# Kernel optimization log

Hardware: AMD Instinct MI355X
Metric: run time of the kernel (lower is better)

The kernel has to match this reference:

```python
import jax, jax.numpy as jnp
import numpy as np

TAU = 2.0          # gumbel-softmax temperature (module default)
NUM_GROUPS = 2
NUM_VARS = 320
EPS = 1e-7


def setup_inputs() -> dict:
    key = jax.random.key(0)
    k1, k2, k3, k4 = jax.random.split(key, 4)
    B, S, D = 32, 2048, 512
    GK = NUM_GROUPS * NUM_VARS            # 640
    dpg = 256 // NUM_GROUPS               # codevector_dim // num_groups = 128
    hidden_states = jax.random.normal(k1, (B, S, D), dtype=jnp.float32)
    mask_time_indices = jnp.ones((B, S), dtype=bool)
    gumbel_noise = jax.random.gumbel(k2, (B * S * NUM_GROUPS, NUM_VARS), dtype=jnp.float32)
    W = jax.random.normal(k3, (GK, D), dtype=jnp.float32) * (1.0 / np.sqrt(D))
    b = jnp.zeros((GK,), dtype=jnp.float32)
    codevectors = jax.random.uniform(k4, (1, GK, dpg), dtype=jnp.float32)
    return {"hidden_states": hidden_states, "mask_time_indices": mask_time_indices,
            "gumbel_noise": gumbel_noise, "W": W, "b": b, "codevectors": codevectors}


def reference(hidden_states, mask_time_indices, gumbel_noise, W, b, codevectors):
    B, S, D = hidden_states.shape
    G, K = NUM_GROUPS, NUM_VARS
    N = B * S

    # linear projection to logits: (B,S,G*K)
    logits = jnp.einsum('bsd,kd->bsk', hidden_states, W) + b
    logits_flat = logits.reshape(N * G, K)

    # training path: gumbel-softmax with hard straight-through
    y_soft = jax.nn.softmax((logits_flat + gumbel_noise) / TAU, axis=-1)
    idx = jnp.argmax(y_soft, axis=-1)
    y_hard = jax.nn.one_hot(idx, K, dtype=y_soft.dtype)
    probs = y_hard + y_soft - jax.lax.stop_gradient(y_soft)   # (N*G, K)

    # perplexity over the plain (no-gumbel) softmax distribution
    soft_dist = jax.nn.softmax(logits_flat.reshape(N, G, K), axis=-1)
    m = mask_time_indices.reshape(-1)[:, None, None]
    marginal = jnp.where(m, soft_dist, 0.0).sum(axis=0) / mask_time_indices.sum()   # (G, K)
    perplexity = jnp.exp(-jnp.sum(marginal * jnp.log(marginal + EPS), axis=-1)).sum()

    # weighted sum of codevectors per group (avoids (N, G*K, d) intermediate)
    cv = codevectors.reshape(G, K, -1)                         # (G, K, d/G)
    out = jnp.einsum('ngk,gkd->ngd', probs.reshape(N, G, K), cv).reshape(B, S, -1)
    return out, perplexity
```

## Files before the change

### kernel.cpp

```cpp
#include <hip/hip_runtime.h>


#define GG   2
#define KK   320
#define NN   65536
#define DD   512
#define DPG  128
#define EPSL 1e-7f
#define NCPY 8
#define BUFB 24576

typedef __attribute__((ext_vector_type(8))) short bf16x8;
typedef __attribute__((ext_vector_type(4))) float f32x4;
typedef __attribute__((address_space(1))) void glb_void;
typedef __attribute__((address_space(3))) void lds_void;

static __device__ __forceinline__ unsigned short f2bf_rne(float f) {
    unsigned u = __float_as_uint(f);
    u += 0x7FFFu + ((u >> 16) & 1u);
    return (unsigned short)(u >> 16);
}

static __device__ __forceinline__ bf16x8 pack8_rne(float4 v0, float4 v1) {
    union { unsigned short s[8]; bf16x8 b; } u;
    u.s[0] = f2bf_rne(v0.x); u.s[1] = f2bf_rne(v0.y);
    u.s[2] = f2bf_rne(v0.z); u.s[3] = f2bf_rne(v0.w);
    u.s[4] = f2bf_rne(v1.x); u.s[5] = f2bf_rne(v1.y);
    u.s[6] = f2bf_rne(v1.z); u.s[7] = f2bf_rne(v1.w);
    return u.b;
}

static __device__ __forceinline__ unsigned ordf(float f) {
    unsigned u = __float_as_uint(f);
    return (u & 0x80000000u) ? ~u : (u | 0x80000000u);
}

__global__ __launch_bounds__(256) void prep_all(
    const float* __restrict__ H, short* __restrict__ Hbf,
    const float* __restrict__ W, short* __restrict__ Wf,
    float* __restrict__ marg, const int* __restrict__ mask,
    float* __restrict__ cnt_out, int* __restrict__ done)
{
    const int b = blockIdx.x, tid = threadIdx.x;
    if (b < 16384) {
        const int F = b * 4 + (tid >> 6);
        const int l = tid & 63;
        const int tile = F >> 5, f = F & 31;
        const int rf = f >> 4, t = f & 15;
        const int row = tile * 32 + rf * 16 + (l >> 2);
        const float* src = H + (size_t)row * DD + t * 32 + (l & 3) * 8;
        float4 v0 = *(const float4*)src;
        float4 v1 = *(const float4*)(src + 4);
        union { unsigned short s[8]; int d[4]; } u;
        u.s[0] = f2bf_rne(v0.x); u.s[1] = f2bf_rne(v0.y);
        u.s[2] = f2bf_rne(v0.z); u.s[3] = f2bf_rne(v0.w);
        u.s[4] = f2bf_rne(v1.x); u.s[5] = f2bf_rne(v1.y);
        u.s[6] = f2bf_rne(v1.z); u.s[7] = f2bf_rne(v1.w);
        const int ls4 = (4 * (l & 15) + (l >> 4)) * 4;
        int4 o;
        o.x = __builtin_amdgcn_ds_bpermute(ls4, u.d[0]);
        o.y = __builtin_amdgcn_ds_bpermute(ls4, u.d[1]);
        o.z = __builtin_amdgcn_ds_bpermute(ls4, u.d[2]);
        o.w = __builtin_amdgcn_ds_bpermute(ls4, u.d[3]);
        *(int4*)(Hbf + (size_t)F * 512 + (size_t)l * 8) = o;
    } else if (b < 16544) {
        int gt = (b - 16384) * 256 + tid;
        int w  = gt >> 6, l = gt & 63;
        int col = 16 * (w >> 4) + (l & 15);
        int k0  = 32 * (w & 15) + 8 * (l >> 4);
        const float* src = W + (size_t)col * DD + k0;
        float4 v0 = *(const float4*)(src);
        float4 v1 = *(const float4*)(src + 4);
        *(bf16x8*)(Wf + (size_t)w * 512 + (size_t)l * 8) = pack8_rne(v0, v1);
    } else {
        __shared__ float red[256];
        for (int i = tid; i < NCPY * GG * KK; i += 256) marg[i] = 0.f;
        if (tid == 0) *done = 0;
        int c = 0;
        for (int n = tid; n < NN; n += 256) c += (mask[n] != 0) ? 1 : 0;
        red[tid] = (float)c;
        __syncthreads();
        for (int s = 128; s > 0; s >>= 1) {
            if (tid < s) red[tid] += red[tid + s];
            __syncthreads();
        }
        if (tid == 0) *cnt_out = red[0];
    }
}

__global__ __launch_bounds__(512, 4) void vq_main(
    const short* Hbf, const int* __restrict__ mask,
    const float* __restrict__ gumbel, const short* __restrict__ Wf,
    const float* __restrict__ bias, const float* __restrict__ cv,
    int* __restrict__ idxW, float* marg,
    int fused, float* __restrict__ out,
    const float* __restrict__ cnt_in, int* done, float* __restrict__ perp_out)
{
    __shared__ __align__(16) char smem[3 * BUFB];
    __shared__ float    red_s[256];
    __shared__ unsigned red_k[256];
    __shared__ float    wrowS[64];
    __shared__ int      idxf[64];
    __shared__ int      lastflag;

    const int tid = threadIdx.x;
    const int l   = tid & 63, wid = tid >> 6;
    const int rh  = wid >> 2, hc = wid & 3;
    const int g   = blockIdx.x & 1;
    const int T   = blockIdx.x >> 1;
    const int n0  = T * 64;
    const int q   = l >> 4,  ln = l & 15;

    const short* gsrc0[3];
#pragma unroll
    for (int j = 0; j < 3; ++j) {
        const int k = wid * 3 + j;
        if (k < 4) gsrc0[j] = Hbf + (size_t)((2 * T + (k >> 1)) * 32 + (k & 1) * 16) * 512 + (size_t)l * 8;
        else       gsrc0[j] = Wf  + (size_t)((g * 20 + (k - 4)) * 16) * 512 + (size_t)l * 8;
    }

#define ISSUE(t_, b_)                                                          \
    { _Pragma("unroll")                                                        \
      for (int j = 0; j < 3; ++j) {                                            \
          const int k = wid * 3 + j;                                           \
          const short* gsrc = (const short*)((const char*)gsrc0[j] + ((t_) << 10)); \
          char* ldst = smem + (b_)*BUFB + k * 1024;                            \
          __builtin_amdgcn_global_load_lds((const glb_void*)gsrc, (lds_void*)ldst, 16, 0, 0); \
      } }

    f32x4 acc[2][5];
    const f32x4 vzero = {0.f, 0.f, 0.f, 0.f};
#pragma unroll
    for (int a = 0; a < 2; ++a)
#pragma unroll
        for (int b = 0; b < 5; ++b) acc[a][b] = vzero;

#define COMPUTE(b_)                                                            \
    { const char* bb_ = smem + (b_)*BUFB;                                      \
      bf16x8 Ar[2], Br[5];                                                     \
      _Pragma("unroll")                                                        \
      for (int rf = 0; rf < 2; ++rf)                                           \
          Ar[rf] = *(const bf16x8*)(bb_ + (rh * 2 + rf) * 1024 + l * 16);      \
      _Pragma("unroll")                                                        \
      for (int cf = 0; cf < 5; ++cf)                                           \
          Br[cf] = *(const bf16x8*)(bb_ + 4096 + (hc * 5 + cf) * 1024 + l * 16); \
      __builtin_amdgcn_s_setprio(1);                                           \
      _Pragma("unroll")                                                        \
      for (int cf = 0; cf < 5; ++cf) {                                         \
          acc[0][cf] = __builtin_amdgcn_mfma_f32_16x16x32_bf16(Ar[0], Br[cf], acc[0][cf], 0, 0, 0); \
          acc[1][cf] = __builtin_amdgcn_mfma_f32_16x16x32_bf16(Ar[1], Br[cf], acc[1][cf], 0, 0, 0); } \
      __builtin_amdgcn_s_setprio(0); }

    ISSUE(0, 0)
#pragma unroll 1
    for (int c = 0; c < 15; ++c) {
        ISSUE(c + 1, (c + 1) % 3)
        asm volatile("s_waitcnt vmcnt(3)" ::: "memory");
        __builtin_amdgcn_sched_barrier(0);
        __builtin_amdgcn_s_barrier();
        COMPUTE(c % 3)
    }
    asm volatile("s_waitcnt vmcnt(0)" ::: "memory");
    __builtin_amdgcn_sched_barrier(0);
    __builtin_amdgcn_s_barrier();
    COMPUTE(0)

    float bb[5];
#pragma unroll
    for (int cf = 0; cf < 5; ++cf) bb[cf] = bias[g * KK + hc * 80 + 16 * cf + ln];

    float gum[8][5];
#pragma unroll
    for (int rf = 0; rf < 2; ++rf)
#pragma unroll
        for (int reg = 0; reg < 4; ++reg) {
            const int row = 32 * rh + 16 * rf + 4 * q + reg;
            const float* gp = gumbel + ((size_t)(n0 + row) * GG + g) * KK + hc * 80 + ln;
#pragma unroll
            for (int cf = 0; cf < 5; ++cf) gum[rf * 4 + reg][cf] = gp[16 * cf];
        }
    __builtin_amdgcn_sched_barrier(0);

#pragma unroll
    for (int cf = 0; cf < 5; ++cf)
#pragma unroll
        for (int rf = 0; rf < 2; ++rf) {
            acc[rf][cf][0] += bb[cf]; acc[rf][cf][1] += bb[cf];
            acc[rf][cf][2] += bb[cf]; acc[rf][cf][3] += bb[cf];
        }

#pragma unroll
    for (int rf = 0; rf < 2; ++rf) {
#pragma unroll
        for (int reg = 0; reg < 4; ++reg) {
            const int row = 32 * rh + 16 * rf + 4 * q + reg;
            float s = 0.f, zm = -3.0e38f;
            int zi = 0;
#pragma unroll
            for (int cf = 0; cf < 5; ++cf) {
                float v = acc[rf][cf][reg];
                float z = v + gum[rf * 4 + reg][cf];
                if (z > zm) { zm = z; zi = hc * 80 + 16 * cf + ln; }
                float e = __expf(v);
                s += e;
                acc[rf][cf][reg] = e;
            }
            unsigned key = (ordf(zm) & 0xFFFFFE00u) | (unsigned)(511 - zi);
#pragma unroll
            for (int d = 1; d <= 8; d <<= 1) {
                s += __shfl_xor(s, d);
                unsigned ko = (unsigned)__shfl_xor((int)key, d);
                key = key > ko ? key : ko;
            }
            if (ln == 0) {
                const int base = row * 4 + hc;
                red_s[base] = s;
                red_k[base] = key;
            }
        }
    }
    __syncthreads();

    if (tid < 64) {
        const int b0 = tid * 4;
        float Z = red_s[b0] + red_s[b0 + 1] + red_s[b0 + 2] + red_s[b0 + 3];
        unsigned km = red_k[b0];
        km = km > red_k[b0 + 1] ? km : red_k[b0 + 1];
        km = km > red_k[b0 + 2] ? km : red_k[b0 + 2];
        km = km > red_k[b0 + 3] ? km : red_k[b0 + 3];
        const int ib = 511 - (int)(km & 511u);
        idxf[tid]  = ib;
        if (!fused) idxW[(size_t)(n0 + tid) * GG + g] = ib;
        wrowS[tid] = ((mask[n0 + tid] != 0) ? 1.0f : 0.0f) / Z;
    }
    __syncthreads();

    float cs[5] = {0.f, 0.f, 0.f, 0.f, 0.f};
#pragma unroll
    for (int rf = 0; rf < 2; ++rf) {
#pragma unroll
        for (int reg = 0; reg < 4; ++reg) {
            const int row = 32 * rh + 16 * rf + 4 * q + reg;
            const float wv = wrowS[row];
#pragma unroll
            for (int cf = 0; cf < 5; ++cf)
                cs[cf] += acc[rf][cf][reg] * wv;
        }
    }
    {
        float* mc = marg + (size_t)(blockIdx.x & (NCPY - 1)) * (GG * KK);
#pragma unroll
        for (int cf = 0; cf < 5; ++cf) {
            float v = cs[cf];
            v += __shfl_xor(v, 16);
            v += __shfl_xor(v, 32);
            if (l < 16) atomicAdd(&mc[g * KK + hc * 80 + 16 * cf + l], v);
        }
    }

    if (fused) {
#pragma unroll
        for (int i = 0; i < 4; ++i) {
            const int e = tid + 512 * i;
            const int row = e >> 5, d4 = e & 31;
            const float4 v = ((const float4*)cv)[((size_t)g * KK + idxf[row]) * 32 + d4];
            ((float4*)(out + (size_t)(n0 + row) * 256 + g * DPG))[d4] = v;
        }
    }

    asm volatile("s_waitcnt vmcnt(0)" ::: "memory");
    __syncthreads();
    if (tid == 0) {
        int old = atomicAdd(done, 1);
        lastflag = (old == 2047) ? 1 : 0;
    }
    __syncthreads();
    if (lastflag) {
        const float invc = 1.0f / cnt_in[0];
        float hg[GG];
#pragma unroll
        for (int gg = 0; gg < GG; ++gg) {
            float h = 0.f;
            for (int c = tid; c < KK; c += 512) {
                float m = 0.f;
#pragma unroll
                for (int x = 0; x < NCPY; ++x)
                    m += atomicAdd(&marg[x * (GG * KK) + gg * KK + c], 0.0f);
                m *= invc;
                h += m * logf(m + EPSL);
            }
#pragma unroll
            for (int d = 1; d < 64; d <<= 1) h += __shfl_xor(h, d);
            if (l == 0) red_s[wid] = h;
            __syncthreads();
            if (tid == 0) {
                float t = 0.f;
                for (int wv = 0; wv < 8; ++wv) t += red_s[wv];
                red_s[64 + gg] = t;
            }
            __syncthreads();
            hg[gg] = red_s[64 + gg];
        }
        if (tid == 0) perp_out[0] = expf(-hg[0]) + expf(-hg[1]);
    }
}

__global__ __launch_bounds__(256) void gather_kernel(
    const int* __restrict__ idxW, const float* __restrict__ cv,
    float* __restrict__ out)
{
    const int e = blockIdx.x * 256 + threadIdx.x;
    const int n = e >> 6, s4 = e & 63, g = s4 >> 5, d4 = s4 & 31;
    const int idx = idxW[(size_t)n * GG + g];
    const float4 v = ((const float4*)cv)[((size_t)g * KK + idx) * 32 + d4];
    ((float4*)out)[e] = v;
}

extern "C" void kernel_launch(void* const* d_in, const int* in_sizes, int n_in,
                              void* d_out, int out_size, void* d_ws, size_t ws_size,
                              hipStream_t stream)
{
    const float* H      = (const float*)d_in[0];
    const int*   mask   = (const int*)d_in[1];
    const float* gumbel = (const float*)d_in[2];
    const float* W      = (const float*)d_in[3];
    const float* bias   = (const float*)d_in[4];
    const float* cv     = (const float*)d_in[5];

    float*  out  = (float*)d_out;
    float*  marg = (float*)d_ws;
    float*  cnt  = (float*)((char*)d_ws + 24576);
    int*    done = (int*)((char*)d_ws + 24580);
    short*  Wf   = (short*)((char*)d_ws + 32768);
    int*    idxW = (int*)((char*)d_ws + 32768 + 655360);

    const size_t hbf_off  = 2 * 1024 * 1024;
    const size_t hbf_need = hbf_off + (size_t)64 * 1024 * 1024;
    const int fused = (ws_size >= hbf_need) ? 1 : 0;
    short* Hbf = fused ? (short*)((char*)d_ws + hbf_off) : (short*)d_out;

    prep_all<<<16545, 256, 0, stream>>>(H, Hbf, W, Wf, marg, mask, cnt, done);
    vq_main<<<2048, 512, 0, stream>>>(Hbf, mask, gumbel, Wf, bias, cv, idxW, marg,
                                      fused, out, cnt, done,
                                      out + (size_t)NN * GG * DPG);
    if (!fused)
        gather_kernel<<<16384, 256, 0, stream>>>(idxW, cv, out);
}
```

Measured before the change: 164.7 us.

## Store bf16 hidden states row-major and gather MFMA fragments with strided loads

```diff
diff --git a/kernel.cpp b/kernel.cpp
--- a/kernel.cpp
+++ b/kernel.cpp
@@ -43,26 +43,10 @@
 {
     const int b = blockIdx.x, tid = threadIdx.x;
     if (b < 16384) {
-        const int F = b * 4 + (tid >> 6);
-        const int l = tid & 63;
-        const int tile = F >> 5, f = F & 31;
-        const int rf = f >> 4, t = f & 15;
-        const int row = tile * 32 + rf * 16 + (l >> 2);
-        const float* src = H + (size_t)row * DD + t * 32 + (l & 3) * 8;
-        float4 v0 = *(const float4*)src;
-        float4 v1 = *(const float4*)(src + 4);
-        union { unsigned short s[8]; int d[4]; } u;
-        u.s[0] = f2bf_rne(v0.x); u.s[1] = f2bf_rne(v0.y);
-        u.s[2] = f2bf_rne(v0.z); u.s[3] = f2bf_rne(v0.w);
-        u.s[4] = f2bf_rne(v1.x); u.s[5] = f2bf_rne(v1.y);
-        u.s[6] = f2bf_rne(v1.z); u.s[7] = f2bf_rne(v1.w);
-        const int ls4 = (4 * (l & 15) + (l >> 4)) * 4;
-        int4 o;
-        o.x = __builtin_amdgcn_ds_bpermute(ls4, u.d[0]);
-        o.y = __builtin_amdgcn_ds_bpermute(ls4, u.d[1]);
-        o.z = __builtin_amdgcn_ds_bpermute(ls4, u.d[2]);
-        o.w = __builtin_amdgcn_ds_bpermute(ls4, u.d[3]);
-        *(int4*)(Hbf + (size_t)F * 512 + (size_t)l * 8) = o;
+        const size_t base = ((size_t)b * 256 + tid) * 8;
+        float4 v0 = *(const float4*)(H + base);
+        float4 v1 = *(const float4*)(H + base + 4);
+        *(bf16x8*)(Hbf + base) = pack8_rne(v0, v1);
     } else if (b < 16544) {
         int gt = (b - 16384) * 256 + tid;
         int w  = gt >> 6, l = gt & 63;
@@ -76,8 +60,13 @@
         __shared__ float red[256];
         for (int i = tid; i < NCPY * GG * KK; i += 256) marg[i] = 0.f;
         if (tid == 0) *done = 0;
+        const int4* m4 = (const int4*)mask;
         int c = 0;
-        for (int n = tid; n < NN; n += 256) c += (mask[n] != 0) ? 1 : 0;
+#pragma unroll 4
+        for (int i = tid; i < NN / 4; i += 256) {
+            int4 v = m4[i];
+            c += (v.x != 0) + (v.y != 0) + (v.z != 0) + (v.w != 0);
+        }
         red[tid] = (float)c;
         __syncthreads();
         for (int s = 128; s > 0; s >>= 1) {
@@ -112,18 +101,24 @@
     const int q   = l >> 4,  ln = l & 15;
 
     const short* gsrc0[3];
+    int stepB[3];
 #pragma unroll
     for (int j = 0; j < 3; ++j) {
         const int k = wid * 3 + j;
-        if (k < 4) gsrc0[j] = Hbf + (size_t)((2 * T + (k >> 1)) * 32 + (k & 1) * 16) * 512 + (size_t)l * 8;
-        else       gsrc0[j] = Wf  + (size_t)((g * 20 + (k - 4)) * 16) * 512 + (size_t)l * 8;
+        if (k < 4) {
+            gsrc0[j] = Hbf + (size_t)(n0 + 16 * k + (l & 15)) * 512 + 8 * (l >> 4);
+            stepB[j] = 64;
+        } else {
+            gsrc0[j] = Wf + (size_t)((g * 20 + (k - 4)) * 16) * 512 + (size_t)l * 8;
+            stepB[j] = 1024;
+        }
     }
 
 #define ISSUE(t_, b_)                                                          \
     { _Pragma("unroll")                                                        \
       for (int j = 0; j < 3; ++j) {                                            \
           const int k = wid * 3 + j;                                           \
-          const short* gsrc = (const short*)((const char*)gsrc0[j] + ((t_) << 10)); \
+          const short* gsrc = (const short*)((const char*)gsrc0[j] + (t_) * stepB[j]); \
           char* ldst = smem + (b_)*BUFB + k * 1024;                            \
           __builtin_amdgcn_global_load_lds((const glb_void*)gsrc, (lds_void*)ldst, 16, 0, 0); \
       } }
```

Result: faster. 132.3 us, median of 3 (-19.7%).
